# Performance work log

Measured on AMD Instinct MI355X. Metric: run time of the kernel, lower is better.

The kernel has to match this reference:

```python
import jax, jax.numpy as jnp
import numpy as np

HIDDEN = 1024
HEADS = 16
MEM = 2
D_H = HIDDEN // HEADS
NEG = -1.0e9


def setup_inputs() -> dict:
    key = jax.random.key(0)
    ks = jax.random.split(key, 8)
    B, M, N = 16, 512, 512
    s = 1.0 / np.sqrt(HIDDEN)
    return {
        "x": jax.random.normal(ks[0], (B, M, HIDDEN), dtype=jnp.float32),
        "y": jax.random.normal(ks[1], (B, N, HIDDEN), dtype=jnp.float32),
        "mask_x": jax.random.randint(ks[2], (B, M), 0, 2, dtype=jnp.int64),
        "mask_y": jax.random.randint(ks[3], (B, N), 0, 2, dtype=jnp.int64),
        "Wx": jax.random.normal(ks[4], (HIDDEN, HIDDEN), dtype=jnp.float32) * s,
        "Wy": jax.random.normal(ks[5], (HIDDEN, HIDDEN), dtype=jnp.float32) * s,
        "x_memory": jax.random.normal(ks[6], (MEM, HIDDEN), dtype=jnp.float32),
        "y_memory": jax.random.normal(ks[7], (MEM, HIDDEN), dtype=jnp.float32),
    }


def _project(t, mem, W):
    # prepend memory tokens, then linear (torch Linear: t @ W^T), split heads
    B = t.shape[0]
    t_mem = jnp.concatenate([jnp.broadcast_to(mem[None], (B, MEM, HIDDEN)), t], axis=1)
    proj = t_mem @ W.T
    proj = proj.reshape(B, t_mem.shape[1], HEADS, D_H)
    return t_mem, proj


def reference(x, y, mask_x, mask_y, Wx, Wy, x_memory, y_memory):
    B = x.shape[0]
    mem_mask = jnp.ones((B, MEM), dtype=mask_x.dtype)
    mx = jnp.concatenate([mem_mask, mask_x], axis=1)  # [B, M+MEM]
    my = jnp.concatenate([mem_mask, mask_y], axis=1)  # [B, N+MEM]

    X_mem, X_proj = _project(x, x_memory, Wx)  # [B,Mm,H], [B,Mm,heads,d_h]
    Y_mem, Y_proj = _project(y, y_memory, Wy)

    # affinity: [B, heads, Mm, Nm]
    aff = jnp.einsum("bmhd,bnhd->bhmn", X_proj, Y_proj)
    aff = jnp.where(mx[:, None, :, None] == 0, NEG, aff)
    aff = jnp.where(my[:, None, None, :] == 0, NEG, aff)

    attn_X = jnp.mean(jax.nn.softmax(aff, axis=2), axis=1)  # [B, Mm, Nm]
    attn_Y = jnp.mean(jax.nn.softmax(aff, axis=3), axis=1)  # [B, Mm, Nm]

    X_in_Y = jnp.einsum("bmn,bmh->bnh", attn_X, X_mem)[:, MEM:, :]  # [B, N, H]
    Y_in_X = jnp.einsum("bmn,bnh->bmh", attn_Y, Y_mem)[:, MEM:, :]  # [B, M, H]
    return X_in_Y, Y_in_X
```

## Files before the change

kernel.cpp:

```cpp
#include <hip/hip_runtime.h>

#define B_   16
#define SEQ  512
#define MM   514
#define HID  1024
#define NH   16
#define DH   64
#define KP   544
#define MTOT (B_ * MM)
#define UNI  (1.0f/514.0f)

typedef unsigned short us;
typedef __attribute__((ext_vector_type(4))) float f32x4;
typedef __attribute__((ext_vector_type(8))) short short8;
typedef __attribute__((ext_vector_type(8))) _Float16 half8;

__device__ __forceinline__ us f2bf(float f) {
  unsigned int u = __float_as_uint(f);
  u = (u + 0x7FFFu + ((u >> 16) & 1u)) >> 16;
  return (us)u;
}
__device__ __forceinline__ float bf2f(us h) {
  return __uint_as_float(((unsigned int)h) << 16);
}
__device__ __forceinline__ us f2h(float f) {
  _Float16 h = (_Float16)f;
  return *(us*)&h;
}
__device__ __forceinline__ unsigned cvt_pk_bf16(float lo, float hi) {
  unsigned d;
  asm("v_cvt_pk_bf16_f32 %0, %1, %2" : "=v"(d) : "v"(lo), "v"(hi));
  return d;
}

__global__ __launch_bounds__(256) void prepack(
    const float* __restrict__ x, const float* __restrict__ y,
    const float* __restrict__ xm, const float* __restrict__ ym,
    const float* __restrict__ Wx, const float* __restrict__ Wy,
    us* __restrict__ Abf, us* __restrict__ Wbf) {
  const int tid = threadIdx.x;
  const int row = blockIdx.x * 4 + (tid >> 6);
  const int path = blockIdx.y;
  const int lane = tid & 63;
  const float* src;
  us* dst;
  if (row < MTOT) {
    const int gb = row / MM, gt = row - gb * MM;
    const float* tin = path ? y : x;
    const float* mv  = path ? ym : xm;
    src = (gt < 2) ? (mv + (size_t)gt * HID)
                   : (tin + ((size_t)(gb * SEQ + gt - 2)) * HID);
    dst = Abf + ((size_t)(path * MTOT + row)) * HID;
  } else {
    const int o = row - MTOT;
    src = (path ? Wy : Wx) + (size_t)o * HID;
    dst = Wbf + ((size_t)(path * HID + o)) * HID;
  }
  const float* s = src + lane * 16;
  f32x4 v0 = *(const f32x4*)(s);
  f32x4 v1 = *(const f32x4*)(s + 4);
  f32x4 v2 = *(const f32x4*)(s + 8);
  f32x4 v3 = *(const f32x4*)(s + 12);
  uint4 w0, w1;
  w0.x = cvt_pk_bf16(v0[0], v0[1]);  w0.y = cvt_pk_bf16(v0[2], v0[3]);
  w0.z = cvt_pk_bf16(v1[0], v1[1]);  w0.w = cvt_pk_bf16(v1[2], v1[3]);
  w1.x = cvt_pk_bf16(v2[0], v2[1]);  w1.y = cvt_pk_bf16(v2[2], v2[3]);
  w1.z = cvt_pk_bf16(v3[0], v3[1]);  w1.w = cvt_pk_bf16(v3[2], v3[3]);
  *(uint4*)(dst + lane * 16)     = w0;
  *(uint4*)(dst + lane * 16 + 8) = w1;
}

__global__ __launch_bounds__(256) void proj_fused2(
    const us* __restrict__ Abf, const us* __restrict__ Wbf,
    us* __restrict__ Px, us* __restrict__ Py) {
  const int lin = blockIdx.x + 8 * (blockIdx.y + 65 * blockIdx.z);
  const int work = (lin & 7) * 130 + (lin >> 3);
  const int path = (work >= 520) ? 1 : 0;
  const int wrem = work - path * 520;
  const int mt = wrem >> 3, nt = wrem & 7;
  us* P = path ? Py : Px;
  const us* Ab = Abf + (size_t)path * MTOT * HID;
  const us* Wb = Wbf + (size_t)path * HID * HID;

  __shared__ __align__(16) us As[128 * 40];
  __shared__ __align__(16) us Bs[128 * 40];
  const int tid = threadIdx.x;
  const int lane = tid & 63, wave = tid >> 6;
  const int c = lane & 15, q = lane >> 4;
  const int wr = wave >> 1, wc = wave & 1;

  const int srow = tid >> 1, sch = (tid & 1) * 16;
  const int grow = mt * 128 + srow;
  const us* asrc = (grow < MTOT) ? (Ab + (size_t)grow * HID + sch) : nullptr;
  const us* bsrc = Wb + (size_t)(nt * 128 + srow) * HID + sch;
  us* wAp = &As[srow * 40 + sch];
  us* wBp = &Bs[srow * 40 + sch];
  const us* rA = &As[(wr * 64 + c) * 40 + q * 8];
  const us* rB = &Bs[(wc * 64 + c) * 40 + q * 8];

  f32x4 acc[4][4];
#pragma unroll
  for (int i = 0; i < 4; i++)
#pragma unroll
    for (int j = 0; j < 4; j++) acc[i][j] = (f32x4){0.f, 0.f, 0.f, 0.f};

  uint4 z4 = {0u, 0u, 0u, 0u};
  uint4 pa0 = z4, pa1 = z4, pb0, pb1;
  if (asrc) { pa0 = *(const uint4*)asrc; pa1 = *(const uint4*)(asrc + 8); }
  pb0 = *(const uint4*)bsrc; pb1 = *(const uint4*)(bsrc + 8);

  for (int kk = 0; kk < HID; kk += 32) {
    __syncthreads();
    *(uint4*)wAp       = pa0;
    *(uint4*)(wAp + 8) = pa1;
    *(uint4*)wBp       = pb0;
    *(uint4*)(wBp + 8) = pb1;
    __syncthreads();
    if (kk + 32 < HID) {
      if (asrc) {
        pa0 = *(const uint4*)(asrc + kk + 32);
        pa1 = *(const uint4*)(asrc + kk + 32 + 8);
      }
      pb0 = *(const uint4*)(bsrc + kk + 32);
      pb1 = *(const uint4*)(bsrc + kk + 32 + 8);
    }
    short8 a[4], bb[4];
#pragma unroll
    for (int i = 0; i < 4; i++) a[i] = *(const short8*)(rA + i * 16 * 40);
#pragma unroll
    for (int j = 0; j < 4; j++) bb[j] = *(const short8*)(rB + j * 16 * 40);
#pragma unroll
    for (int i = 0; i < 4; i++)
#pragma unroll
      for (int j = 0; j < 4; j++)
        acc[i][j] = __builtin_amdgcn_mfma_f32_16x16x32_bf16(a[i], bb[j], acc[i][j], 0, 0, 0);
  }
#pragma unroll
  for (int i = 0; i < 4; i++) {
#pragma unroll
    for (int r = 0; r < 4; r++) {
      int gr = mt * 128 + wr * 64 + i * 16 + q * 4 + r;
      if (gr < MTOT) {
        size_t rb = (size_t)(path * MTOT + gr) * HID - (size_t)path * MTOT * HID;
        rb = (size_t)gr * HID;
#pragma unroll
        for (int j = 0; j < 4; j++)
          P[rb + nt * 128 + wc * 64 + j * 16 + c] = f2bf(acc[i][j][r]);
      }
    }
  }
}

__device__ __forceinline__ void stage_bf(
    us* Xs, const us* P, int b, int r0, int h, int tid) {
#pragma unroll
  for (int i = 0; i < 2; i++) {
    int idx = tid + i * 256;
    int row = idx >> 3, qq = idx & 7;
    *(uint4*)&Xs[row * 72 + qq * 8] =
        *(const uint4*)(P + ((size_t)(b * MM + min(r0 + row, MM - 1))) * HID + h * DH + qq * 8);
  }
}

__global__ __launch_bounds__(512) void sums_big(
    const us* __restrict__ Px, const us* __restrict__ Py,
    const int* __restrict__ mx, const int* __restrict__ my,
    float* __restrict__ Sums) {
  const int half = blockIdx.x, h = blockIdx.y, b = blockIdx.z;
  const int NCH = half ? 5 : 4;
  const int n0 = half * 256;
  __shared__ __align__(16) us Ys[320 * 72];
  __shared__ __align__(16) us Xs[64 * 72];
  __shared__ float cS[320];
  __shared__ int myS[320];
  __shared__ int mxS[576];
  const int tid = threadIdx.x;
  const int lane = tid & 63, wave = tid >> 6;
  const int c = lane & 15, q = lane >> 4;
  const int strip = wave & 3, cgrp = wave >> 2;
  const int chm = (NCH + 1) >> 1;
  const int ch0 = cgrp ? chm : 0;
  const int ch1 = cgrp ? NCH : chm;

  for (int i = tid; i < 320; i += 512) {
    cS[i] = 0.f;
    int n = n0 + i;
    myS[i] = (n >= MM) ? 0 : ((n < 2) ? 1 : my[b * SEQ + n - 2]);
  }
  for (int i = tid; i < 576; i += 512)
    mxS[i] = (i >= MM) ? 0 : ((i < 2) ? 1 : mx[b * SEQ + i - 2]);
  {
    const int row8 = tid >> 3, qq = tid & 7;
    for (int it = 0; it < NCH; it++) {
      int row = it * 64 + row8;
      int grow = min(n0 + row, MM - 1);
      *(uint4*)&Ys[row * 72 + qq * 8] =
          *(const uint4*)(Py + ((size_t)(b * MM + grow)) * HID + h * DH + qq * 8);
    }
  }
  __syncthreads();

  const size_t base = ((size_t)(b * NH + h)) * MM;
  const size_t COLOFF = (size_t)B_ * NH * MM;

  for (int mt = 0; mt < 9; mt++) {
    {
      const int row8 = tid >> 3, qq = tid & 7;
      int grow = min(mt * 64 + row8, MM - 1);
      *(uint4*)&Xs[row8 * 72 + qq * 8] =
          *(const uint4*)(Px + ((size_t)(b * MM + grow)) * HID + h * DH + qq * 8);
    }
    __syncthreads();
    short8 a0 = *(const short8*)&Xs[(strip * 16 + c) * 72 + q * 8];
    short8 a1 = *(const short8*)&Xs[(strip * 16 + c) * 72 + q * 8 + 32];
    int rm[4];
#pragma unroll
    for (int r = 0; r < 4; r++) rm[r] = mxS[mt * 64 + strip * 16 + q * 4 + r];
    float rowp[4] = {0.f, 0.f, 0.f, 0.f};
    for (int ch = ch0; ch < ch1; ch++) {
#pragma unroll
      for (int ss = 0; ss < 4; ss++) {
        int nloc = ch * 64 + ss * 16 + c;
        short8 b0 = *(const short8*)&Ys[nloc * 72 + q * 8];
        short8 b1 = *(const short8*)&Ys[nloc * 72 + q * 8 + 32];
        f32x4 av = (f32x4){0.f, 0.f, 0.f, 0.f};
        av = __builtin_amdgcn_mfma_f32_16x16x32_bf16(a0, b0, av, 0, 0, 0);
        av = __builtin_amdgcn_mfma_f32_16x16x32_bf16(a1, b1, av, 0, 0, 0);
        int cmv = myS[nloc];
        float colp = 0.f;
#pragma unroll
        for (int r = 0; r < 4; r++) {
          float e = (rm[r] && cmv) ? __expf(av[r]) : 0.f;
          rowp[r] += e;
          colp += e;
        }
        colp += __shfl_xor(colp, 16);
        colp += __shfl_xor(colp, 32);
        if (q == 0) atomicAdd(&cS[nloc], colp);
      }
    }
#pragma unroll
    for (int d = 1; d < 16; d <<= 1)
#pragma unroll
      for (int r = 0; r < 4; r++) rowp[r] += __shfl_xor(rowp[r], d, 16);
    if (c == 0) {
#pragma unroll
      for (int r = 0; r < 4; r++) {
        int m = mt * 64 + strip * 16 + q * 4 + r;
        if (m < MM) atomicAdd(&Sums[base + m], rowp[r]);
      }
    }
    __syncthreads();
  }
  for (int i = tid; i < NCH * 64; i += 512) {
    int n = n0 + i;
    if (n < MM) Sums[COLOFF + base + n] = cS[i];
  }
}

__global__ __launch_bounds__(256) void inv_kernel(float* __restrict__ Sums) {
  int i = blockIdx.x * 256 + threadIdx.x;
  if (i < 2 * B_ * NH * MM) {
    float s = Sums[i];
    Sums[i] = (s > 0.f) ? (1.f / s) : -1.f;
  }
}

__global__ __launch_bounds__(256) void attn_mfma2(
    const us* __restrict__ Px, const us* __restrict__ Py,
    const int* __restrict__ mx, const int* __restrict__ my,
    const float* __restrict__ Inv,
    us* __restrict__ attnXT, us* __restrict__ attnY) {
  const int nt = blockIdx.x, mt = blockIdx.y, b = blockIdx.z;
  __shared__ __align__(16) us Xs[64 * 72];
  __shared__ __align__(16) us Ys[64 * 72];
  const int tid = threadIdx.x;
  const int lane = tid & 63, wave = tid >> 6;
  const int c = lane & 15, q = lane >> 4;
  const size_t COLOFF = (size_t)B_ * NH * MM;

  int mreg[4], rm[4], ncol[4], cm[4];
#pragma unroll
  for (int r = 0; r < 4; r++) {
    mreg[r] = mt * 64 + wave * 16 + q * 4 + r;
    rm[r] = (mreg[r] >= MM) ? 0 : ((mreg[r] < 2) ? 1 : mx[b * SEQ + mreg[r] - 2]);
  }
#pragma unroll
  for (int s = 0; s < 4; s++) {
    ncol[s] = nt * 64 + s * 16 + c;
    cm[s] = (ncol[s] >= MM) ? 0 : ((ncol[s] < 2) ? 1 : my[b * SEQ + ncol[s] - 2]);
  }

  float aX[4][4], aY[4][4];
#pragma unroll
  for (int s = 0; s < 4; s++)
#pragma unroll
    for (int r = 0; r < 4; r++) { aX[s][r] = 0.f; aY[s][r] = 0.f; }

  for (int h = 0; h < NH; h++) {
    __syncthreads();
    stage_bf(Xs, Px, b, mt * 64, h, tid);
    stage_bf(Ys, Py, b, nt * 64, h, tid);
    __syncthreads();
    short8 a0 = *(const short8*)&Xs[(wave * 16 + c) * 72 + q * 8];
    short8 a1 = *(const short8*)&Xs[(wave * 16 + c) * 72 + q * 8 + 32];
    const size_t base = ((size_t)(b * NH + h)) * MM;
    float invR[4];
#pragma unroll
    for (int r = 0; r < 4; r++) invR[r] = Inv[base + min(mreg[r], MM - 1)];
#pragma unroll
    for (int s = 0; s < 4; s++) {
      float invC = Inv[COLOFF + base + min(ncol[s], MM - 1)];
      short8 b0 = *(const short8*)&Ys[(s * 16 + c) * 72 + q * 8];
      short8 b1 = *(const short8*)&Ys[(s * 16 + c) * 72 + q * 8 + 32];
      f32x4 av = (f32x4){0.f, 0.f, 0.f, 0.f};
      av = __builtin_amdgcn_mfma_f32_16x16x32_bf16(a0, b0, av, 0, 0, 0);
      av = __builtin_amdgcn_mfma_f32_16x16x32_bf16(a1, b1, av, 0, 0, 0);
#pragma unroll
      for (int r = 0; r < 4; r++) {
        float e = (rm[r] && cm[s]) ? __expf(av[r]) : 0.f;
        aY[s][r] += (invR[r] < 0.f) ? UNI : e * invR[r];
        aX[s][r] += (invC < 0.f) ? UNI : e * invC;
      }
    }
  }
#pragma unroll
  for (int s = 0; s < 4; s++) {
    if (ncol[s] < MM) {
      us* xrow = attnXT + ((size_t)(b * MM + ncol[s])) * KP;
      if (mreg[3] < MM) {
        uint2 w;
        w.x = (unsigned)f2h(aX[s][0] * 0.0625f) | ((unsigned)f2h(aX[s][1] * 0.0625f) << 16);
        w.y = (unsigned)f2h(aX[s][2] * 0.0625f) | ((unsigned)f2h(aX[s][3] * 0.0625f) << 16);
        *(uint2*)&xrow[mreg[0]] = w;
      } else {
#pragma unroll
        for (int r = 0; r < 4; r++)
          if (mreg[r] < MM) xrow[mreg[r]] = f2h(aX[s][r] * 0.0625f);
      }
#pragma unroll
      for (int r = 0; r < 4; r++)
        if (mreg[r] < MM)
          attnY[((size_t)(b * MM + mreg[r])) * KP + ncol[s]] = f2h(aY[s][r] * 0.0625f);
    }
  }
}

__global__ __launch_bounds__(256) void transpose_fused(
    const float* __restrict__ x, const float* __restrict__ y,
    const float* __restrict__ xm, const float* __restrict__ ym,
    us* __restrict__ XTx, us* __restrict__ XTy) {
  const int kt = blockIdx.x, ot = blockIdx.y;
  const int b = blockIdx.z & 15, path = blockIdx.z >> 4;
  const float* tin  = path ? y  : x;
  const float* mvec = path ? ym : xm;
  us* XT            = path ? XTy : XTx;
  __shared__ __align__(16) us T[64 * 40];
  const int tid = threadIdx.x;
  {
    const int row = tid >> 3;
    const int col8 = (tid & 7) * 8;
    const int kg = kt * 32 + row;
    const float* src = (kg < 2) ? (mvec + (size_t)kg * HID + ot * 64 + col8)
                     : (kg < MM) ? (tin + ((size_t)(b * SEQ + kg - 2)) * HID + ot * 64 + col8)
                                 : nullptr;
    f32x4 v0 = (f32x4){0.f, 0.f, 0.f, 0.f};
    f32x4 v1 = (f32x4){0.f, 0.f, 0.f, 0.f};
    if (src) { v0 = *(const f32x4*)src; v1 = *(const f32x4*)(src + 4); }
#pragma unroll
    for (int j = 0; j < 4; j++) T[(col8 + j) * 40 + row] = f2h(v0[j]);
#pragma unroll
    for (int j = 0; j < 4; j++) T[(col8 + 4 + j) * 40 + row] = f2h(v1[j]);
  }
  __syncthreads();
  const int orow = tid >> 2, kc = (tid & 3) * 8;
  uint4 w = *(const uint4*)&T[orow * 40 + kc];
  *(uint4*)&XT[((size_t)(b * HID + ot * 64 + orow)) * KP + kt * 32 + kc] = w;
}

__global__ __launch_bounds__(256) void outg_fused(
    const us* __restrict__ A0, const us* __restrict__ A1,
    const us* __restrict__ XTx, const us* __restrict__ XTy,
    float* __restrict__ outp) {
  const int ot = blockIdx.x, rt = blockIdx.y;
  const int b = blockIdx.z & 15, path = blockIdx.z >> 4;
  const us* A  = path ? A1 : A0;
  const us* XT = path ? XTy : XTx;
  float* op = outp + (path ? (size_t)B_ * SEQ * HID : 0);
  const int r0 = rt * 128, o0 = ot * 128;
  __shared__ __align__(16) us As[128 * 40];
  __shared__ __align__(16) us Bs[128 * 40];
  const int tid = threadIdx.x;
  const int lane = tid & 63, wave = tid >> 6;
  const int c = lane & 15, q = lane >> 4;
  const int wr = wave >> 1, wc = wave & 1;

  const int srow = tid >> 2, sch = (tid & 3) * 8;
  const us* gA0 = A + ((size_t)(b * MM + 2 + r0 + srow)) * KP + sch;
  const us* gA1 = gA0 + (size_t)64 * KP;
  const us* gB0 = XT + ((size_t)(b * HID + o0 + srow)) * KP + sch;
  const us* gB1 = gB0 + (size_t)64 * KP;
  us* wA0 = &As[srow * 40 + sch];
  us* wA1 = wA0 + 64 * 40;
  us* wB0 = &Bs[srow * 40 + sch];
  us* wB1 = wB0 + 64 * 40;

  f32x4 acc[4][4];
#pragma unroll
  for (int i = 0; i < 4; i++)
#pragma unroll
    for (int j = 0; j < 4; j++) acc[i][j] = (f32x4){0.f, 0.f, 0.f, 0.f};

  const us* rA = &As[(wr * 64 + c) * 40 + q * 8];
  const us* rB = &Bs[(wc * 64 + c) * 40 + q * 8];

  uint4 pA0 = *(const uint4*)gA0;
  uint4 pA1 = *(const uint4*)gA1;
  uint4 pB0 = *(const uint4*)gB0;
  uint4 pB1 = *(const uint4*)gB1;

  for (int kk = 0; kk < KP; kk += 32) {
    __syncthreads();
    *(uint4*)wA0 = pA0;
    *(uint4*)wA1 = pA1;
    *(uint4*)wB0 = pB0;
    *(uint4*)wB1 = pB1;
    __syncthreads();
    if (kk + 32 < KP) {
      pA0 = *(const uint4*)(gA0 + kk + 32);
      pA1 = *(const uint4*)(gA1 + kk + 32);
      pB0 = *(const uint4*)(gB0 + kk + 32);
      pB1 = *(const uint4*)(gB1 + kk + 32);
    }
    half8 a[4], bb[4];
#pragma unroll
    for (int i = 0; i < 4; i++) a[i] = *(const half8*)(rA + i * 16 * 40);
#pragma unroll
    for (int j = 0; j < 4; j++) bb[j] = *(const half8*)(rB + j * 16 * 40);
#pragma unroll
    for (int i = 0; i < 4; i++)
#pragma unroll
      for (int j = 0; j < 4; j++)
        acc[i][j] = __builtin_amdgcn_mfma_f32_16x16x32_f16(a[i], bb[j], acc[i][j], 0, 0, 0);
  }
#pragma unroll
  for (int i = 0; i < 4; i++) {
#pragma unroll
    for (int rr = 0; rr < 4; rr++) {
      int r = r0 + wr * 64 + i * 16 + q * 4 + rr;
      size_t rowbase = ((size_t)(b * SEQ + r)) * HID;
#pragma unroll
      for (int j = 0; j < 4; j++)
        op[rowbase + o0 + wc * 64 + j * 16 + c] = acc[i][j][rr];
    }
  }
}

__global__ __launch_bounds__(256) void attn_mfma_old(
    const us* __restrict__ Px, const us* __restrict__ Py,
    const int* __restrict__ mx, const int* __restrict__ my,
    const float* __restrict__ Inv,
    us* __restrict__ attnX, us* __restrict__ attnY,
    const int doX, const int doY) {
  const int nt = blockIdx.x, mt = blockIdx.y, b = blockIdx.z;
  __shared__ __align__(16) us Xs[64 * 72];
  __shared__ __align__(16) us Ys[64 * 72];
  const int tid = threadIdx.x;
  const int lane = tid & 63, wave = tid >> 6;
  const int c = lane & 15, q = lane >> 4;
  const size_t COLOFF = (size_t)B_ * NH * MM;

  int mreg[4], rm[4], ncol[4], cm[4];
#pragma unroll
  for (int r = 0; r < 4; r++) {
    mreg[r] = mt * 64 + wave * 16 + q * 4 + r;
    rm[r] = (mreg[r] >= MM) ? 0 : ((mreg[r] < 2) ? 1 : mx[b * SEQ + mreg[r] - 2]);
  }
#pragma unroll
  for (int s = 0; s < 4; s++) {
    ncol[s] = nt * 64 + s * 16 + c;
    cm[s] = (ncol[s] >= MM) ? 0 : ((ncol[s] < 2) ? 1 : my[b * SEQ + ncol[s] - 2]);
  }

  float aX[4][4], aY[4][4];
#pragma unroll
  for (int s = 0; s < 4; s++)
#pragma unroll
    for (int r = 0; r < 4; r++) { aX[s][r] = 0.f; aY[s][r] = 0.f; }

  for (int h = 0; h < NH; h++) {
    __syncthreads();
    stage_bf(Xs, Px, b, mt * 64, h, tid);
    stage_bf(Ys, Py, b, nt * 64, h, tid);
    __syncthreads();
    short8 a0 = *(const short8*)&Xs[(wave * 16 + c) * 72 + q * 8];
    short8 a1 = *(const short8*)&Xs[(wave * 16 + c) * 72 + q * 8 + 32];
    const size_t base = ((size_t)(b * NH + h)) * MM;
    float invR[4];
#pragma unroll
    for (int r = 0; r < 4; r++) invR[r] = Inv[base + min(mreg[r], MM - 1)];
#pragma unroll
    for (int s = 0; s < 4; s++) {
      float invC = Inv[COLOFF + base + min(ncol[s], MM - 1)];
      short8 b0 = *(const short8*)&Ys[(s * 16 + c) * 72 + q * 8];
      short8 b1 = *(const short8*)&Ys[(s * 16 + c) * 72 + q * 8 + 32];
      f32x4 av = (f32x4){0.f, 0.f, 0.f, 0.f};
      av = __builtin_amdgcn_mfma_f32_16x16x32_bf16(a0, b0, av, 0, 0, 0);
      av = __builtin_amdgcn_mfma_f32_16x16x32_bf16(a1, b1, av, 0, 0, 0);
#pragma unroll
      for (int r = 0; r < 4; r++) {
        float e = (rm[r] && cm[s]) ? __expf(av[r]) : 0.f;
        aY[s][r] += (invR[r] < 0.f) ? UNI : e * invR[r];
        aX[s][r] += (invC < 0.f) ? UNI : e * invC;
      }
    }
  }
#pragma unroll
  for (int s = 0; s < 4; s++) {
#pragma unroll
    for (int r = 0; r < 4; r++) {
      if (mreg[r] < MM && ncol[s] < MM) {
        size_t idx = ((size_t)(b * MM + mreg[r])) * MM + ncol[s];
        if (doX) attnX[idx] = f2bf(aX[s][r] * 0.0625f);
        if (doY) attnY[idx] = f2bf(aY[s][r] * 0.0625f);
      }
    }
  }
}

__global__ __launch_bounds__(256) void outg_kernel(
    const us* __restrict__ attn, const float* __restrict__ tin,
    const float* __restrict__ mvec, float* __restrict__ outp, const int trans) {
  const int otile = blockIdx.x, rtile = blockIdx.y, b = blockIdx.z;
  __shared__ __align__(16) float Ss[32 * 132];
  __shared__ __align__(16) float Ms[32 * 132];
  const int tid = threadIdx.x;
  const int r0 = rtile * 128, o0 = otile * 128;

  float acc[8][8];
#pragma unroll
  for (int i = 0; i < 8; i++)
#pragma unroll
    for (int j = 0; j < 8; j++) acc[i][j] = 0.f;

  for (int kk = 0; kk < 544; kk += 32) {
    __syncthreads();
    if (trans) {
      int rq = (tid & 31) * 4;
      int kr = tid >> 5;
#pragma unroll
      for (int kb = 0; kb < 32; kb += 8) {
        int k = kr + kb;
        int kg = kk + k;
        if (kg < MM) {
          const us* src = attn + ((size_t)(b * MM + kg)) * MM + 2 + r0 + rq;
          Ss[k * 132 + rq + 0] = bf2f(src[0]);
          Ss[k * 132 + rq + 1] = bf2f(src[1]);
          Ss[k * 132 + rq + 2] = bf2f(src[2]);
          Ss[k * 132 + rq + 3] = bf2f(src[3]);
        } else {
          Ss[k * 132 + rq + 0] = 0.f;
          Ss[k * 132 + rq + 1] = 0.f;
          Ss[k * 132 + rq + 2] = 0.f;
          Ss[k * 132 + rq + 3] = 0.f;
        }
      }
    } else {
      int r = tid >> 1;
      int kh = (tid & 1) * 16;
      const us* src = attn + ((size_t)(b * MM + 2 + r0 + r)) * MM;
#pragma unroll
      for (int j = 0; j < 16; j++) {
        int k = kh + j;
        int kg = kk + k;
        Ss[k * 132 + r] = (kg < MM) ? bf2f(src[kg]) : 0.f;
      }
    }
    {
      int k = tid >> 3;
      int oq = (tid & 7) * 16;
      int kg = kk + k;
      const float* mr = (kg < 2) ? (mvec + (size_t)kg * HID)
                      : (kg < MM) ? (tin + ((size_t)(b * SEQ + kg - 2)) * HID)
                                  : nullptr;
#pragma unroll
      for (int qq = 0; qq < 4; qq++) {
        f32x4 v = (f32x4){0.f, 0.f, 0.f, 0.f};
        if (mr) v = *(const f32x4*)(mr + o0 + oq + qq * 4);
        *(f32x4*)&Ms[k * 132 + oq + qq * 4] = v;
      }
    }
    __syncthreads();
    const int ty = tid >> 4, tx = tid & 15;
    for (int k = 0; k < 32; k++) {
      f32x4 s0 = *(const f32x4*)&Ss[k * 132 + ty * 4];
      f32x4 s1 = *(const f32x4*)&Ss[k * 132 + 64 + ty * 4];
      f32x4 m0 = *(const f32x4*)&Ms[k * 132 + tx * 4];
      f32x4 m1 = *(const f32x4*)&Ms[k * 132 + 64 + tx * 4];
#pragma unroll
      for (int i = 0; i < 4; i++) {
#pragma unroll
        for (int j = 0; j < 4; j++) {
          acc[i][j]         += s0[i] * m0[j];
          acc[i][j + 4]     += s0[i] * m1[j];
          acc[i + 4][j]     += s1[i] * m0[j];
          acc[i + 4][j + 4] += s1[i] * m1[j];
        }
      }
    }
  }
  const int ty = tid >> 4, tx = tid & 15;
#pragma unroll
  for (int ri = 0; ri < 2; ri++) {
#pragma unroll
    for (int i = 0; i < 4; i++) {
      int r = r0 + ri * 64 + ty * 4 + i;
      size_t rowbase = ((size_t)(b * SEQ + r)) * HID;
#pragma unroll
      for (int oi = 0; oi < 2; oi++) {
        int o = o0 + oi * 64 + tx * 4;
        f32x4 v;
#pragma unroll
        for (int j = 0; j < 4; j++) v[j] = acc[ri * 4 + i][oi * 4 + j];
        *(f32x4*)&outp[rowbase + o] = v;
      }
    }
  }
}

extern "C" void kernel_launch(void* const* d_in, const int* in_sizes, int n_in,
                              void* d_out, int out_size, void* d_ws, size_t ws_size,
                              hipStream_t stream) {
  const float* x  = (const float*)d_in[0];
  const float* y  = (const float*)d_in[1];
  const int* mask_x = (const int*)d_in[2];
  const int* mask_y = (const int*)d_in[3];
  const float* Wx = (const float*)d_in[4];
  const float* Wy = (const float*)d_in[5];
  const float* xm = (const float*)d_in[6];
  const float* ym = (const float*)d_in[7];
  float* out = (float*)d_out;

  const size_t szSums = (size_t)2 * B_ * NH * MM * 4;
  const size_t szP    = (size_t)B_ * MM * HID * 2;
  const size_t szAtt  = (size_t)B_ * MM * MM * 2;
  const size_t szAttP = (size_t)B_ * MM * KP * 2;
  const size_t szXT   = (size_t)B_ * HID * KP * 2;
  const size_t R_off  = szSums + 2 * szAttP;
  const size_t needNew = R_off + 2 * szXT;

  char* ws = (char*)d_ws;

  us* Abf = (us*)d_out;
  us* Wbf = (us*)d_out + (size_t)2 * MTOT * HID;

  if (ws_size >= needNew) {
    float* Sums = (float*)ws;
    us* A0  = (us*)(ws + szSums);
    us* A1  = (us*)(ws + szSums + szAttP);
    us* Px  = (us*)(ws + R_off);
    us* Py  = (us*)(ws + R_off + szP);
    us* XTx = (us*)(ws + R_off);
    us* XTy = (us*)(ws + R_off + szXT);

    prepack<<<dim3((MTOT + HID) / 4, 2), 256, 0, stream>>>(x, y, xm, ym, Wx, Wy, Abf, Wbf);
    proj_fused2<<<dim3(8, 65, 2), 256, 0, stream>>>(Abf, Wbf, Px, Py);
    hipMemsetAsync(Sums, 0, szSums, stream);
    hipMemsetAsync(A0, 0, 2 * szAttP, stream);
    sums_big<<<dim3(2, 16, 16), 512, 0, stream>>>(Px, Py, mask_x, mask_y, Sums);
    inv_kernel<<<dim3((2 * B_ * NH * MM + 255) / 256), 256, 0, stream>>>(Sums);
    attn_mfma2<<<dim3(9, 9, 16), 256, 0, stream>>>(Px, Py, mask_x, mask_y, Sums, A0, A1);
    transpose_fused<<<dim3(17, 16, 32), 256, 0, stream>>>(x, y, xm, ym, XTx, XTy);
    outg_fused<<<dim3(8, 4, 32), 256, 0, stream>>>(A0, A1, XTx, XTy, out);
    return;
  }

  const int dual = (ws_size >= szSums + 2 * szP + 2 * szAtt) ? 1 : 0;
  float* Sums = (float*)(ws);
  us* Px = (us*)(ws + szSums);
  us* Py = (us*)(ws + szSums + szP);
  us* A0 = (us*)(ws + szSums + 2 * szP);
  us* A1 = dual ? (us*)(ws + szSums + 2 * szP + szAtt) : A0;

  prepack<<<dim3((MTOT + HID) / 4, 2), 256, 0, stream>>>(x, y, xm, ym, Wx, Wy, Abf, Wbf);
  proj_fused2<<<dim3(8, 65, 2), 256, 0, stream>>>(Abf, Wbf, Px, Py);
  hipMemsetAsync(Sums, 0, szSums, stream);
  sums_big<<<dim3(2, 16, 16), 512, 0, stream>>>(Px, Py, mask_x, mask_y, Sums);
  inv_kernel<<<dim3((2 * B_ * NH * MM + 255) / 256), 256, 0, stream>>>(Sums);

  if (dual) {
    attn_mfma_old<<<dim3(9, 9, 16), 256, 0, stream>>>(Px, Py, mask_x, mask_y, Sums, A0, A1, 1, 1);
    outg_kernel<<<dim3(8, 4, 16), 256, 0, stream>>>(A0, x, xm, out, 1);
    outg_kernel<<<dim3(8, 4, 16), 256, 0, stream>>>(A1, y, ym, out + (size_t)B_ * SEQ * HID, 0);
  } else {
    attn_mfma_old<<<dim3(9, 9, 16), 256, 0, stream>>>(Px, Py, mask_x, mask_y, Sums, A0, A0, 1, 0);
    outg_kernel<<<dim3(8, 4, 16), 256, 0, stream>>>(A0, x, xm, out, 1);
    attn_mfma_old<<<dim3(9, 9, 16), 256, 0, stream>>>(Px, Py, mask_x, mask_y, Sums, A0, A0, 0, 1);
    outg_kernel<<<dim3(8, 4, 16), 256, 0, stream>>>(A0, y, ym, out + (size_t)B_ * SEQ * HID, 0);
  }
}
```

Baseline: 373.2 us.

## Split sums kernel over row segments and enlarge attention tiles to 128x128

The column/row sum kernel now splits its 9 row tiles into 3 segments across extra blocks, so column sums are accumulated with global atomics instead of plain stores. This raises parallelism from 512 to 1536 blocks. The attention kernel switches from 64x64 tiles with 256 threads to 128x128 tiles with 512 threads, giving each wave a 64x32 sub-tile. That cuts the redundant restaging of Px/Py per head and improves operand reuse, at the cost of more registers per thread and more padded work at the 514 boundary.

```diff
diff --git a/kernel.cpp b/kernel.cpp
--- a/kernel.cpp
+++ b/kernel.cpp
@@ -141,8 +141,7 @@
     for (int r = 0; r < 4; r++) {
       int gr = mt * 128 + wr * 64 + i * 16 + q * 4 + r;
       if (gr < MTOT) {
-        size_t rb = (size_t)(path * MTOT + gr) * HID - (size_t)path * MTOT * HID;
-        rb = (size_t)gr * HID;
+        size_t rb = (size_t)gr * HID;
 #pragma unroll
         for (int j = 0; j < 4; j++)
           P[rb + nt * 128 + wc * 64 + j * 16 + c] = f2bf(acc[i][j][r]);
@@ -166,7 +165,8 @@
     const us* __restrict__ Px, const us* __restrict__ Py,
     const int* __restrict__ mx, const int* __restrict__ my,
     float* __restrict__ Sums) {
-  const int half = blockIdx.x, h = blockIdx.y, b = blockIdx.z;
+  const int sx = blockIdx.x, h = blockIdx.y, b = blockIdx.z;
+  const int half = sx & 1, seg = sx >> 1;
   const int NCH = half ? 5 : 4;
   const int n0 = half * 256;
   __shared__ __align__(16) us Ys[320 * 72];
@@ -203,7 +203,7 @@
   const size_t base = ((size_t)(b * NH + h)) * MM;
   const size_t COLOFF = (size_t)B_ * NH * MM;
 
-  for (int mt = 0; mt < 9; mt++) {
+  for (int mt = seg * 3; mt < seg * 3 + 3; mt++) {
     {
       const int row8 = tid >> 3, qq = tid & 7;
       int grow = min(mt * 64 + row8, MM - 1);
@@ -254,7 +254,7 @@
   }
   for (int i = tid; i < NCH * 64; i += 512) {
     int n = n0 + i;
-    if (n < MM) Sums[COLOFF + base + n] = cS[i];
+    if (n < MM) atomicAdd(&Sums[COLOFF + base + n], cS[i]);
   }
 }
 
@@ -266,82 +266,118 @@
   }
 }
 
-__global__ __launch_bounds__(256) void attn_mfma2(
+__global__ __launch_bounds__(512) void attn_big(
     const us* __restrict__ Px, const us* __restrict__ Py,
     const int* __restrict__ mx, const int* __restrict__ my,
     const float* __restrict__ Inv,
     us* __restrict__ attnXT, us* __restrict__ attnY) {
   const int nt = blockIdx.x, mt = blockIdx.y, b = blockIdx.z;
-  __shared__ __align__(16) us Xs[64 * 72];
-  __shared__ __align__(16) us Ys[64 * 72];
+  __shared__ __align__(16) us Xs[128 * 72];
+  __shared__ __align__(16) us Ys[128 * 72];
   const int tid = threadIdx.x;
   const int lane = tid & 63, wave = tid >> 6;
   const int c = lane & 15, q = lane >> 4;
+  const int wr = wave >> 2, wn = wave & 3;
   const size_t COLOFF = (size_t)B_ * NH * MM;
 
-  int mreg[4], rm[4], ncol[4], cm[4];
-#pragma unroll
-  for (int r = 0; r < 4; r++) {
-    mreg[r] = mt * 64 + wave * 16 + q * 4 + r;
-    rm[r] = (mreg[r] >= MM) ? 0 : ((mreg[r] < 2) ? 1 : mx[b * SEQ + mreg[r] - 2]);
-  }
-#pragma unroll
-  for (int s = 0; s < 4; s++) {
-    ncol[s] = nt * 64 + s * 16 + c;
+  const int mrow0 = mt * 128 + wr * 64 + q * 4;
+  unsigned rmask = 0;
+#pragma unroll
+  for (int i = 0; i < 4; i++)
+#pragma unroll
+    for (int r = 0; r < 4; r++) {
+      int m = mrow0 + i * 16 + r;
+      int v = (m >= MM) ? 0 : ((m < 2) ? 1 : mx[b * SEQ + m - 2]);
+      rmask |= (unsigned)(v != 0) << (i * 4 + r);
+    }
+  int ncol[2], cm[2];
+#pragma unroll
+  for (int s = 0; s < 2; s++) {
+    ncol[s] = nt * 128 + wn * 32 + s * 16 + c;
     cm[s] = (ncol[s] >= MM) ? 0 : ((ncol[s] < 2) ? 1 : my[b * SEQ + ncol[s] - 2]);
   }
 
-  float aX[4][4], aY[4][4];
-#pragma unroll
-  for (int s = 0; s < 4; s++)
-#pragma unroll
-    for (int r = 0; r < 4; r++) { aX[s][r] = 0.f; aY[s][r] = 0.f; }
+  float aX[2][4][4], aY[2][4][4];
+#pragma unroll
+  for (int s = 0; s < 2; s++)
+#pragma unroll
+    for (int i = 0; i < 4; i++)
+#pragma unroll
+      for (int r = 0; r < 4; r++) { aX[s][i][r] = 0.f; aY[s][i][r] = 0.f; }
 
   for (int h = 0; h < NH; h++) {
     __syncthreads();
-    stage_bf(Xs, Px, b, mt * 64, h, tid);
-    stage_bf(Ys, Py, b, nt * 64, h, tid);
-    __syncthreads();
-    short8 a0 = *(const short8*)&Xs[(wave * 16 + c) * 72 + q * 8];
-    short8 a1 = *(const short8*)&Xs[(wave * 16 + c) * 72 + q * 8 + 32];
+    {
+      const int row = tid >> 2;
+      const int qq = (tid & 3) * 2;
+      const us* px = Px + ((size_t)(b * MM + min(mt * 128 + row, MM - 1))) * HID + h * DH;
+      const us* py = Py + ((size_t)(b * MM + min(nt * 128 + row, MM - 1))) * HID + h * DH;
+      *(uint4*)&Xs[row * 72 + qq * 8]       = *(const uint4*)(px + qq * 8);
+      *(uint4*)&Xs[row * 72 + (qq + 1) * 8] = *(const uint4*)(px + (qq + 1) * 8);
+      *(uint4*)&Ys[row * 72 + qq * 8]       = *(const uint4*)(py + qq * 8);
+      *(uint4*)&Ys[row * 72 + (qq + 1) * 8] = *(const uint4*)(py + (qq + 1) * 8);
+    }
+    __syncthreads();
     const size_t base = ((size_t)(b * NH + h)) * MM;
-    float invR[4];
-#pragma unroll
-    for (int r = 0; r < 4; r++) invR[r] = Inv[base + min(mreg[r], MM - 1)];
-#pragma unroll
-    for (int s = 0; s < 4; s++) {
-      float invC = Inv[COLOFF + base + min(ncol[s], MM - 1)];
-      short8 b0 = *(const short8*)&Ys[(s * 16 + c) * 72 + q * 8];
-      short8 b1 = *(const short8*)&Ys[(s * 16 + c) * 72 + q * 8 + 32];
-      f32x4 av = (f32x4){0.f, 0.f, 0.f, 0.f};
-      av = __builtin_amdgcn_mfma_f32_16x16x32_bf16(a0, b0, av, 0, 0, 0);
-      av = __builtin_amdgcn_mfma_f32_16x16x32_bf16(a1, b1, av, 0, 0, 0);
-#pragma unroll
-      for (int r = 0; r < 4; r++) {
-        float e = (rm[r] && cm[s]) ? __expf(av[r]) : 0.f;
-        aY[s][r] += (invR[r] < 0.f) ? UNI : e * invR[r];
-        aX[s][r] += (invC < 0.f) ? UNI : e * invC;
-      }
-    }
-  }
-#pragma unroll
-  for (int s = 0; s < 4; s++) {
+    float invR[4][4];
+#pragma unroll
+    for (int i = 0; i < 4; i++)
+#pragma unroll
+      for (int r = 0; r < 4; r++)
+        invR[i][r] = Inv[base + min(mrow0 + i * 16 + r, MM - 1)];
+    float invC[2];
+    short8 b0[2], b1[2];
+#pragma unroll
+    for (int s = 0; s < 2; s++) {
+      invC[s] = Inv[COLOFF + base + min(ncol[s], MM - 1)];
+      b0[s] = *(const short8*)&Ys[(wn * 32 + s * 16 + c) * 72 + q * 8];
+      b1[s] = *(const short8*)&Ys[(wn * 32 + s * 16 + c) * 72 + q * 8 + 32];
+    }
+#pragma unroll
+    for (int i = 0; i < 4; i++) {
+      short8 a0 = *(const short8*)&Xs[(wr * 64 + i * 16 + c) * 72 + q * 8];
+      short8 a1 = *(const short8*)&Xs[(wr * 64 + i * 16 + c) * 72 + q * 8 + 32];
+#pragma unroll
+      for (int s = 0; s < 2; s++) {
+        f32x4 av = (f32x4){0.f, 0.f, 0.f, 0.f};
+        av = __builtin_amdgcn_mfma_f32_16x16x32_bf16(a0, b0[s], av, 0, 0, 0);
+        av = __builtin_amdgcn_mfma_f32_16x16x32_bf16(a1, b1[s], av, 0, 0, 0);
+#pragma unroll
+        for (int r = 0; r < 4; r++) {
+          int rmv = (rmask >> (i * 4 + r)) & 1;
+          float e = (rmv && cm[s]) ? __expf(av[r]) : 0.f;
+          aY[s][i][r] += (invR[i][r] < 0.f) ? UNI : e * invR[i][r];
+          aX[s][i][r] += (invC[s] < 0.f) ? UNI : e * invC[s];
+        }
+      }
+    }
+  }
+#pragma unroll
+  for (int s = 0; s < 2; s++) {
     if (ncol[s] < MM) {
       us* xrow = attnXT + ((size_t)(b * MM + ncol[s])) * KP;
-      if (mreg[3] < MM) {
-        uint2 w;
-        w.x = (unsigned)f2h(aX[s][0] * 0.0625f) | ((unsigned)f2h(aX[s][1] * 0.0625f) << 16);
-        w.y = (unsigned)f2h(aX[s][2] * 0.0625f) | ((unsigned)f2h(aX[s][3] * 0.0625f) << 16);
-        *(uint2*)&xrow[mreg[0]] = w;
-      } else {
-#pragma unroll
-        for (int r = 0; r < 4; r++)
-          if (mreg[r] < MM) xrow[mreg[r]] = f2h(aX[s][r] * 0.0625f);
-      }
-#pragma unroll
-      for (int r = 0; r < 4; r++)
-        if (mreg[r] < MM)
-          attnY[((size_t)(b * MM + mreg[r])) * KP + ncol[s]] = f2h(aY[s][r] * 0.0625f);
+#pragma unroll
+      for (int i = 0; i < 4; i++) {
+        int m0 = mrow0 + i * 16;
+        if (m0 + 3 < MM) {
+          uint2 w;
+          w.x = (unsigned)f2h(aX[s][i][0] * 0.0625f) | ((unsigned)f2h(aX[s][i][1] * 0.0625f) << 16);
+          w.y = (unsigned)f2h(aX[s][i][2] * 0.0625f) | ((unsigned)f2h(aX[s][i][3] * 0.0625f) << 16);
+          *(uint2*)&xrow[m0] = w;
+        } else {
+#pragma unroll
+          for (int r = 0; r < 4; r++)
+            if (m0 + r < MM) xrow[m0 + r] = f2h(aX[s][i][r] * 0.0625f);
+        }
+      }
+#pragma unroll
+      for (int i = 0; i < 4; i++)
+#pragma unroll
+        for (int r = 0; r < 4; r++) {
+          int m = mrow0 + i * 16 + r;
+          if (m < MM)
+            attnY[((size_t)(b * MM + m)) * KP + ncol[s]] = f2h(aY[s][i][r] * 0.0625f);
+        }
     }
   }
 }
@@ -667,9 +703,9 @@
     proj_fused2<<<dim3(8, 65, 2), 256, 0, stream>>>(Abf, Wbf, Px, Py);
     hipMemsetAsync(Sums, 0, szSums, stream);
     hipMemsetAsync(A0, 0, 2 * szAttP, stream);
-    sums_big<<<dim3(2, 16, 16), 512, 0, stream>>>(Px, Py, mask_x, mask_y, Sums);
+    sums_big<<<dim3(6, 16, 16), 512, 0, stream>>>(Px, Py, mask_x, mask_y, Sums);
     inv_kernel<<<dim3((2 * B_ * NH * MM + 255) / 256), 256, 0, stream>>>(Sums);
-    attn_mfma2<<<dim3(9, 9, 16), 256, 0, stream>>>(Px, Py, mask_x, mask_y, Sums, A0, A1);
+    attn_big<<<dim3(5, 5, 16), 512, 0, stream>>>(Px, Py, mask_x, mask_y, Sums, A0, A1);
     transpose_fused<<<dim3(17, 16, 32), 256, 0, stream>>>(x, y, xm, ym, XTx, XTy);
     outg_fused<<<dim3(8, 4, 32), 256, 0, stream>>>(A0, A1, XTx, XTy, out);
     return;
@@ -685,7 +721,7 @@
   prepack<<<dim3((MTOT + HID) / 4, 2), 256, 0, stream>>>(x, y, xm, ym, Wx, Wy, Abf, Wbf);
   proj_fused2<<<dim3(8, 65, 2), 256, 0, stream>>>(Abf, Wbf, Px, Py);
   hipMemsetAsync(Sums, 0, szSums, stream);
-  sums_big<<<dim3(2, 16, 16), 512, 0, stream>>>(Px, Py, mask_x, mask_y, Sums);
+  sums_big<<<dim3(6, 16, 16), 512, 0, stream>>>(Px, Py, mask_x, mask_y, Sums);
   inv_kernel<<<dim3((2 * B_ * NH * MM + 255) / 256), 256, 0, stream>>>(Sums);
 
   if (dual) {
```

After: 395.0 us. +5.8%, slower.
